# Optimization experiments

Hardware: AMD Instinct MI355X
Metric: run time of the kernel (lower is better)

## Reference

```python
import jax, jax.numpy as jnp
import numpy as np

BETA = 0.9
T = 16
THR = 1.0
SLOPE = 25.0  # snntorch surrogate.fast_sigmoid default slope


@jax.custom_vjp
def spike(x):
    # Heaviside forward, fast-sigmoid surrogate backward (snntorch fast_sigmoid)
    return (x > 0.0).astype(x.dtype)

def _spike_fwd(x):
    return spike(x), x

def _spike_bwd(x, g):
    return (g / (SLOPE * jnp.abs(x) + 1.0) ** 2,)

spike.defvjp(_spike_fwd, _spike_bwd)


def conv1d(x, w, b, pad):
    # x: (B, C_in, L), w: (C_out, C_in, K)
    y = jax.lax.conv_general_dilated(
        x, w, window_strides=(1,), padding=[(pad, pad)],
        dimension_numbers=("NCH", "OIH", "NCH"))
    return y + b[None, :, None]


def lif(cur, mem):
    # snntorch Leaky, reset_mechanism='subtract', threshold=1.0.
    # reset spike is computed from the PREVIOUS membrane and detached.
    reset = jax.lax.stop_gradient((mem > THR).astype(cur.dtype))
    mem = BETA * mem + cur - reset * THR
    spk = spike(mem - THR)
    return spk, mem


def setup_inputs() -> dict:
    key = jax.random.key(0)
    ks = jax.random.split(key, 14)

    def u(k, shape, fan_in):
        bound = 1.0 / np.sqrt(fan_in)
        return jax.random.uniform(k, shape, jnp.float32, -bound, bound)

    x = jax.random.normal(ks[0], (2048, 2, 128), dtype=jnp.float32)
    W1 = u(ks[1], (256, 2, 5), 2 * 5);    b1 = u(ks[2], (256,), 2 * 5)
    W2 = u(ks[3], (128, 256, 3), 256 * 3); b2 = u(ks[4], (128,), 256 * 3)
    W3 = u(ks[5], (64, 128, 3), 128 * 3);  b3 = u(ks[6], (64,), 128 * 3)
    W4 = u(ks[7], (2, 64, 3), 64 * 3);     b4 = u(ks[8], (2,), 64 * 3)
    fw1 = u(ks[9], (100, 256), 256);       fb1 = u(ks[10], (100,), 256)
    fw2 = u(ks[11], (40, 100), 100);       fb2 = u(ks[12], (40,), 100)
    return {"x": x, "W1": W1, "b1": b1, "W2": W2, "b2": b2,
            "W3": W3, "b3": b3, "W4": W4, "b4": b4,
            "fw1": fw1, "fb1": fb1, "fw2": fw2, "fb2": fb2}


def reference(x, W1, b1, W2, b2, W3, b3, W4, b4, fw1, fb1, fw2, fb2):
    B, _, L = x.shape
    f32 = x.dtype
    # conv1 input is constant across timesteps -> hoist (same math)
    cur1 = conv1d(x, W1, b1, 2)
    init = (jnp.zeros((B, 256, L), f32), jnp.zeros((B, 128, L), f32),
            jnp.zeros((B, 64, L), f32), jnp.zeros((B, 2, L), f32),
            jnp.zeros((B, 100), f32), jnp.zeros((B, 40), f32))

    def step(carry, _):
        m1, m2, m3, m4, m5, acc = carry
        s1, m1 = lif(cur1, m1)
        s2, m2 = lif(conv1d(s1, W2, b2, 1), m2)
        s3, m3 = lif(conv1d(s2, W3, b3, 1), m3)
        s4, m4 = lif(conv1d(s3, W4, b4, 1), m4)
        flat = s4.reshape(B, -1)                      # (B, 256)
        s5, m5 = lif(flat @ fw1.T + fb1, m5)
        acc = acc + s5 @ fw2.T + fb2
        return (m1, m2, m3, m4, m5, acc), None

    (_, _, _, _, _, acc), _ = jax.lax.scan(step, init, None, length=T)
    return acc / T
```

## Files before the change

### kernel.cpp

```cpp
#include <hip/hip_runtime.h>
#include <stdint.h>

#define BETA 0.9f

typedef unsigned short u16;
typedef unsigned char u8;
typedef _Float16 f16x8 __attribute__((ext_vector_type(8)));
typedef float f32x4 __attribute__((ext_vector_type(4)));

__device__ __forceinline__ void async_copy16(const void* g, void* l) {
  __builtin_amdgcn_global_load_lds(
      (const __attribute__((address_space(1))) uint32_t*)g,
      (__attribute__((address_space(3))) uint32_t*)l, 16, 0, 0);
}

__device__ __forceinline__ f16x8 expandB(uint32_t byte) {
  union { uint32_t u[4]; f16x8 v; } r;
  uint32_t z = byte | (byte << 15);
#pragma unroll
  for (int m = 0; m < 4; ++m)
    r.u[m] = ((z >> (2 * m)) & 0x10001u) << 12;
  return r.v;
}

__global__ void prep_kernel(const float* __restrict__ W2, const float* __restrict__ W3,
                            const float* __restrict__ fw1, const float* __restrict__ fw2,
                            u16* __restrict__ A2c, u16* __restrict__ A3c,
                            float* __restrict__ fw1T, float* __restrict__ fw2T) {
  int o = blockIdx.x * 256 + threadIdx.x;
  if (o < 98304) {
    int tap = o >> 15, r = o & 32767, co = r >> 8, ci = r & 255;
    float w = W2[(co * 256 + ci) * 3 + tap];
    float h = (float)(_Float16)w;
    _Float16 hv = (_Float16)(h * 2048.0f);
    _Float16 mv = (_Float16)((w - h) * 2048.0f);
    u16 hb, mb;
    __builtin_memcpy(&hb, &hv, 2);
    __builtin_memcpy(&mb, &mv, 2);
    int c = ci >> 5, cl = ci & 31;
    A2c[(((c * 2 + 0) * 3 + tap) * 128 + co) * 32 + cl] = hb;
    A2c[(((c * 2 + 1) * 3 + tap) * 128 + co) * 32 + cl] = mb;
  }
  int o2 = o - 98304;
  if (o2 >= 0 && o2 < 24576) {
    int tap = o2 >> 13, r = o2 & 8191, co = r >> 7, ci = r & 127;
    float w = W3[(co * 128 + ci) * 3 + tap];
    float h = (float)(_Float16)w;
    _Float16 hv = (_Float16)(h * 2048.0f);
    _Float16 mv = (_Float16)((w - h) * 2048.0f);
    u16 hb, mb;
    __builtin_memcpy(&hb, &hv, 2);
    __builtin_memcpy(&mb, &mv, 2);
    int c = ci >> 5, cl = ci & 31;
    A3c[(((c * 2 + 0) * 3 + tap) * 64 + co) * 32 + cl] = hb;
    A3c[(((c * 2 + 1) * 3 + tap) * 64 + co) * 32 + cl] = mb;
  }
  int o3 = o - (98304 + 24576);
  if (o3 >= 0 && o3 < 25600) {
    int f = o3 / 100, i = o3 % 100;
    fw1T[o3] = fw1[i * 256 + f];
  }
  int o4 = o - (98304 + 24576 + 25600);
  if (o4 >= 0 && o4 < 4000) {
    int i = o4 / 40, j = o4 % 40;
    fw2T[o4] = fw2[j * 100 + i];
  }
}

__global__ __launch_bounds__(256) void conv1_lif_kernel(
    const float* __restrict__ x, const float* __restrict__ W1,
    const float* __restrict__ b1, u8* __restrict__ SBT2) {
  __shared__ float xl[2][132];
  __shared__ u16 bl[8][128];
  int b = blockIdx.x, g = blockIdx.y;
  int tid = threadIdx.x;
  for (int i = tid; i < 264; i += 256) {
    int ci = i / 132, idx = i % 132, lg = idx - 2;
    xl[ci][idx] = (lg >= 0 && lg < 128) ? x[(b * 2 + ci) * 128 + lg] : 0.0f;
  }
  __syncthreads();
  int cosub = tid >> 5, tx = tid & 31;
  int co = g * 8 + cosub;
  float w[2][5];
#pragma unroll
  for (int ci = 0; ci < 2; ++ci)
#pragma unroll
    for (int k = 0; k < 5; ++k) w[ci][k] = W1[(co * 2 + ci) * 5 + k];
  float bias = b1[co];
  float cur[4];
#pragma unroll
  for (int j = 0; j < 4; ++j) {
    float acc = bias;
#pragma unroll
    for (int ci = 0; ci < 2; ++ci)
#pragma unroll
      for (int k = 0; k < 5; ++k) acc += w[ci][k] * xl[ci][4 * tx + j + k];
    cur[j] = acc;
  }
  float m[4] = {0.f, 0.f, 0.f, 0.f}, sp[4] = {0.f, 0.f, 0.f, 0.f};
  uint32_t bits[4] = {0u, 0u, 0u, 0u};
#pragma unroll
  for (int t = 0; t < 16; ++t) {
#pragma unroll
    for (int j = 0; j < 4; ++j) {
      m[j] = BETA * m[j] + cur[j] - sp[j];
      bool s = m[j] > 1.0f;
      bits[j] |= ((uint32_t)s) << t;
      sp[j] = s ? 1.0f : 0.0f;
    }
  }
#pragma unroll
  for (int j = 0; j < 4; ++j) bl[cosub][4 * tx + j] = (u16)bits[j];
  __syncthreads();
  if (tid < 128) {
    int l = tid;
    uint32_t wv[8];
#pragma unroll
    for (int j = 0; j < 8; ++j) wv[j] = bl[j][l];
    uint32_t ov[4];
#pragma unroll
    for (int k = 0; k < 4; ++k) {
      uint32_t v = 0;
#pragma unroll
      for (int tt = 0; tt < 4; ++tt) {
        int t = k * 4 + tt;
        uint32_t by = 0;
#pragma unroll
        for (int j = 0; j < 8; ++j) by |= ((wv[j] >> t) & 1u) << j;
        v |= by << (8 * tt);
      }
      ov[k] = v;
    }
    *(uint4*)(SBT2 + ((size_t)(b * 128 + l) * 32 + g) * 16) =
        make_uint4(ov[0], ov[1], ov[2], ov[3]);
  }
}

template <int CIN, int COUT, bool SBTOUT>
__global__ __launch_bounds__(256, 3) void conv_mfma_kernel(
    const u8* __restrict__ SBT, const u16* __restrict__ Agc,
    const float* __restrict__ bias, void* __restrict__ outp) {
  constexpr int NPHYS = CIN / 32;
  constexpr int NVIRT = 2 * NPHYS;
  constexpr int MT = COUT / 32;
  constexpr int GB = CIN / 8;
  constexpr int ABYTES = 3 * COUT * 32 * 2;
  constexpr int AW = ABYTES / 4;
  constexpr int AISS = AW / 1024;
  constexpr int EPB = 18432 + COUT * 8 * 2;
  constexpr int LDSSZ = (2 * ABYTES > EPB) ? 2 * ABYTES : EPB;
  __shared__ __align__(16) char lds[LDSSZ];

  int b = blockIdx.x, lb = blockIdx.y * 8;
  int tid = threadIdx.x, lane = tid & 63, wid = tid >> 6;
  int wx = wid & 1, wy = wid >> 1;
  int q = lane >> 4, xx = lane & 15;
  int mbase = wy * (COUT / 2);
  int lw = lb + wx * 4;

  f32x4 acc[MT][4];
#pragma unroll
  for (int mt = 0; mt < MT; ++mt)
#pragma unroll
    for (int nt = 0; nt < 4; ++nt) acc[mt][nt] = (f32x4){0.f, 0.f, 0.f, 0.f};

  uint32_t byt[6];
#pragma unroll
  for (int u = 0; u < 6; ++u) {
    int l_in = lw + u - 1;
    byt[u] = ((unsigned)l_in < 128u)
                 ? (uint32_t)SBT[((size_t)(b * 128 + l_in) * GB + q) * 16 + xx]
                 : 0u;
  }
  {
    const char* gsrc = (const char*)Agc + (size_t)wid * AW + lane * 16;
    char* ldst = lds + wid * AW;
#pragma unroll
    for (int i = 0; i < AISS; ++i) async_copy16(gsrc + i * 1024, ldst + i * 1024);
  }

  f16x8 Bf[6];
#pragma unroll 2
  for (int v = 0; v < NVIRT; ++v) {
    __syncthreads();
    if (v + 1 < NVIRT) {
      const char* gsrc = (const char*)Agc + (size_t)(v + 1) * ABYTES +
                         (size_t)wid * AW + lane * 16;
      char* ldst = lds + ((v + 1) & 1) * ABYTES + wid * AW;
#pragma unroll
      for (int i = 0; i < AISS; ++i) async_copy16(gsrc + i * 1024, ldst + i * 1024);
    }
    if ((v & 1) == 0) {
#pragma unroll
      for (int u = 0; u < 6; ++u) Bf[u] = expandB(byt[u]);
      int pn = (v >> 1) + 1;
      if (pn < NPHYS) {
#pragma unroll
        for (int u = 0; u < 6; ++u) {
          int l_in = lw + u - 1;
          byt[u] = ((unsigned)l_in < 128u)
                       ? (uint32_t)SBT[((size_t)(b * 128 + l_in) * GB + pn * 4 + q) * 16 + xx]
                       : 0u;
        }
      }
    }
    const u16* Asv = (const u16*)(lds + (v & 1) * ABYTES);
#pragma unroll
    for (int tap = 0; tap < 3; ++tap)
#pragma unroll
      for (int mt = 0; mt < MT; ++mt) {
        f16x8 Af = *(const f16x8*)(Asv + ((size_t)(tap * COUT + mbase + mt * 16 + xx)) * 32 + q * 8);
#pragma unroll
        for (int nt = 0; nt < 4; ++nt)
          acc[mt][nt] = __builtin_amdgcn_mfma_f32_16x16x32_f16(
              Af, Bf[nt + tap], acc[mt][nt], 0, 0, 0);
      }
  }
  __syncthreads();

  float* scr = (float*)(void*)lds + wid * 1152;
  u16* bl = (u16*)(lds + 18432);
#pragma unroll
  for (int mt = 0; mt < MT; ++mt) {
#pragma unroll
    for (int nt = 0; nt < 4; ++nt)
#pragma unroll
      for (int r = 0; r < 4; ++r)
        scr[(nt * 16 + q * 4 + r) * 18 + xx] = acc[mt][nt][r];
    __syncthreads();
    int co = mbase + mt * 16 + xx;
    float bc = bias[co];
    const float* rowp = scr + (q * 16 + xx) * 18;
    float mm = 0.f, sp = 0.f;
    uint32_t bits = 0;
#pragma unroll
    for (int t = 0; t < 16; ++t) {
      float cur = rowp[t] + bc;
      mm = BETA * mm + cur - sp;
      bool s = mm > 1.0f;
      bits |= ((uint32_t)s) << t;
      sp = s ? 1.0f : 0.0f;
    }
    bl[co * 8 + wx * 4 + q] = (u16)bits;
    __syncthreads();
  }

  if constexpr (SBTOUT) {
    constexpr int GBo = COUT / 8;
    if (tid < GBo * 8) {
      int g = tid & (GBo - 1), ll = tid / GBo;
      uint32_t wv[8];
#pragma unroll
      for (int j = 0; j < 8; ++j) wv[j] = bl[(8 * g + j) * 8 + ll];
      uint32_t ov[4];
#pragma unroll
      for (int k = 0; k < 4; ++k) {
        uint32_t v = 0;
#pragma unroll
        for (int tt = 0; tt < 4; ++tt) {
          int t = k * 4 + tt;
          uint32_t by = 0;
#pragma unroll
          for (int j = 0; j < 8; ++j) by |= ((wv[j] >> t) & 1u) << j;
          v |= by << (8 * tt);
        }
        ov[k] = v;
      }
      *(uint4*)((u8*)outp + ((size_t)(b * 128 + lb + ll) * GBo + g) * 16) =
          make_uint4(ov[0], ov[1], ov[2], ov[3]);
    }
  } else {
    if (tid < COUT) {
      uint4 v = *(const uint4*)(bl + tid * 8);
      *(uint4*)((u16*)outp + ((size_t)b * COUT + tid) * 128 + lb) = v;
    }
  }
}

__global__ __launch_bounds__(256) void head_kernel(
    const u16* __restrict__ s3bits, const float* __restrict__ W4,
    const float* __restrict__ b4, const float* __restrict__ fw1T,
    const float* __restrict__ fb1, const float* __restrict__ fw2T,
    const float* __restrict__ fb2, float* __restrict__ out) {
  __shared__ u16 s3l[64][130];
  __shared__ float W4l[384];
  __shared__ u16 flat4[256];
  __shared__ u16 s5b[100];
  int b = blockIdx.x, tid = threadIdx.x;

  for (int i = tid; i < 64 * 130; i += 256) {
    int ci = i / 130, idx = i % 130, lg = idx - 1;
    s3l[ci][idx] = (lg >= 0 && lg < 128) ? s3bits[((size_t)b * 64 + ci) * 128 + lg] : (u16)0;
  }
  for (int i = tid; i < 384; i += 256) W4l[i] = W4[i];
  __syncthreads();

  {
    int co = tid >> 7, l = tid & 127;
    float acc4[16];
#pragma unroll
    for (int t = 0; t < 16; ++t) acc4[t] = 0.f;
    for (int ci = 0; ci < 64; ++ci) {
#pragma unroll
      for (int k = 0; k < 3; ++k) {
        float wv = W4l[(co * 64 + ci) * 3 + k];
        uint32_t msk = s3l[ci][l + k];
#pragma unroll
        for (int t = 0; t < 16; ++t)
          acc4[t] = fmaf(wv, (float)((msk >> t) & 1u), acc4[t]);
      }
    }
    float bc = b4[co];
    float m = 0.f, sp = 0.f;
    uint32_t bits = 0;
#pragma unroll
    for (int t = 0; t < 16; ++t) {
      m = BETA * m + (acc4[t] + bc) - sp;
      bool s = m > 1.0f;
      bits |= ((uint32_t)s) << t;
      sp = s ? 1.0f : 0.0f;
    }
    flat4[tid] = (u16)bits;
  }
  __syncthreads();

  if (tid < 100) {
    float acc5[16];
#pragma unroll
    for (int t = 0; t < 16; ++t) acc5[t] = 0.f;
    for (int f = 0; f < 256; ++f) {
      float wv = fw1T[f * 100 + tid];
      uint32_t msk = flat4[f];
#pragma unroll
      for (int t = 0; t < 16; ++t)
        acc5[t] = fmaf(wv, (float)((msk >> t) & 1u), acc5[t]);
    }
    float bc = fb1[tid];
    float m = 0.f, sp = 0.f;
    uint32_t bits = 0;
#pragma unroll
    for (int t = 0; t < 16; ++t) {
      m = BETA * m + (acc5[t] + bc) - sp;
      bool s = m > 1.0f;
      bits |= ((uint32_t)s) << t;
      sp = s ? 1.0f : 0.0f;
    }
    s5b[tid] = (u16)bits;
  }
  __syncthreads();

  if (tid < 40) {
    float a = 0.f;
    for (int i = 0; i < 100; ++i) {
      float wv = fw2T[i * 40 + tid];
      a = fmaf(wv, (float)__popc((uint32_t)s5b[i]), a);
    }
    out[b * 40 + tid] = a * 0.0625f + fb2[tid];
  }
}

extern "C" void kernel_launch(void* const* d_in, const int* in_sizes, int n_in,
                              void* d_out, int out_size, void* d_ws, size_t ws_size,
                              hipStream_t stream) {
  const float* x   = (const float*)d_in[0];
  const float* W1  = (const float*)d_in[1];
  const float* b1  = (const float*)d_in[2];
  const float* W2  = (const float*)d_in[3];
  const float* b2  = (const float*)d_in[4];
  const float* W3  = (const float*)d_in[5];
  const float* b3  = (const float*)d_in[6];
  const float* W4  = (const float*)d_in[7];
  const float* b4  = (const float*)d_in[8];
  const float* fw1 = (const float*)d_in[9];
  const float* fb1 = (const float*)d_in[10];
  const float* fw2 = (const float*)d_in[11];
  const float* fb2 = (const float*)d_in[12];
  float* out = (float*)d_out;

  char* ws = (char*)d_ws;
  u16*   A2c  = (u16*)(ws);
  u16*   A3c  = (u16*)(ws + 393216);
  float* fw1T = (float*)(ws + 491520);
  float* fw2T = (float*)(ws + 593920);
  u8*    SBT2 = (u8*)(ws + 610304);
  u8*    SBT3 = (u8*)(ws + 610304 + 134217728);
  u16*   s3b  = (u16*)(ws + 610304 + 134217728 + 67108864);

  prep_kernel<<<dim3(596), dim3(256), 0, stream>>>(W2, W3, fw1, fw2, A2c, A3c, fw1T, fw2T);
  conv1_lif_kernel<<<dim3(2048, 32), dim3(256), 0, stream>>>(x, W1, b1, SBT2);
  conv_mfma_kernel<256, 128, true><<<dim3(2048, 16), dim3(256), 0, stream>>>(SBT2, A2c, b2, SBT3);
  conv_mfma_kernel<128, 64, false><<<dim3(2048, 16), dim3(256), 0, stream>>>(SBT3, A3c, b3, s3b);
  head_kernel<<<dim3(2048), dim3(256), 0, stream>>>(s3b, W4, b4, fw1T, fb1, fw2T, fb2, out);
}
```

Measured before the change: 2.025 ms.

## Switch conv MFMA from split-fp16 to three-limb int8 MFMA with binary spikes

Replaces the two-term fp16 weight split (hi+residual) and f16 MFMA with a three-limb int8 fixed-point decomposition of the weights and i32 16x16x64 int8 MFMA, since spike inputs are 0/1. Accumulators are shifted left by 7 bits between limbs and rescaled by 2^-25 at the end. This doubles the K per MFMA and halves the weight bytes per limb, but now does three passes instead of two and fully unrolls the channel loop. It also repacks spike bytes into int8 lanes and changes the weight layout, and the fixed-point scheme risks precision or overflow differences near the threshold.

```diff
diff --git a/kernel.cpp b/kernel.cpp
--- a/kernel.cpp
+++ b/kernel.cpp
@@ -5,8 +5,8 @@
 
 typedef unsigned short u16;
 typedef unsigned char u8;
-typedef _Float16 f16x8 __attribute__((ext_vector_type(8)));
-typedef float f32x4 __attribute__((ext_vector_type(4)));
+typedef signed char i8;
+typedef int i32x4 __attribute__((ext_vector_type(4)));
 
 __device__ __forceinline__ void async_copy16(const void* g, void* l) {
   __builtin_amdgcn_global_load_lds(
@@ -14,46 +14,39 @@
       (__attribute__((address_space(3))) uint32_t*)l, 16, 0, 0);
 }
 
-__device__ __forceinline__ f16x8 expandB(uint32_t byte) {
-  union { uint32_t u[4]; f16x8 v; } r;
-  uint32_t z = byte | (byte << 15);
-#pragma unroll
-  for (int m = 0; m < 4; ++m)
-    r.u[m] = ((z >> (2 * m)) & 0x10001u) << 12;
-  return r.v;
-}
-
 __global__ void prep_kernel(const float* __restrict__ W2, const float* __restrict__ W3,
                             const float* __restrict__ fw1, const float* __restrict__ fw2,
-                            u16* __restrict__ A2c, u16* __restrict__ A3c,
+                            i8* __restrict__ A2c, i8* __restrict__ A3c,
                             float* __restrict__ fw1T, float* __restrict__ fw2T) {
   int o = blockIdx.x * 256 + threadIdx.x;
   if (o < 98304) {
     int tap = o >> 15, r = o & 32767, co = r >> 8, ci = r & 255;
     float w = W2[(co * 256 + ci) * 3 + tap];
-    float h = (float)(_Float16)w;
-    _Float16 hv = (_Float16)(h * 2048.0f);
-    _Float16 mv = (_Float16)((w - h) * 2048.0f);
-    u16 hb, mb;
-    __builtin_memcpy(&hb, &hv, 2);
-    __builtin_memcpy(&mb, &mv, 2);
-    int c = ci >> 5, cl = ci & 31;
-    A2c[(((c * 2 + 0) * 3 + tap) * 128 + co) * 32 + cl] = hb;
-    A2c[(((c * 2 + 1) * 3 + tap) * 128 + co) * 32 + cl] = mb;
+    float d0 = __builtin_rintf(w * 0x1p11f);
+    float r1 = w - d0 * 0x1p-11f;
+    float d1 = __builtin_rintf(r1 * 0x1p18f);
+    float r2 = r1 - d1 * 0x1p-18f;
+    float d2 = __builtin_rintf(r2 * 0x1p25f);
+    int phys = ci >> 6, cl = ci & 63;
+    int base = ((phys * 3 + tap) * 128 + co) * 64 + cl;
+    A2c[base] = (i8)(int)d0;
+    A2c[98304 + base] = (i8)(int)d1;
+    A2c[196608 + base] = (i8)(int)d2;
   }
   int o2 = o - 98304;
   if (o2 >= 0 && o2 < 24576) {
     int tap = o2 >> 13, r = o2 & 8191, co = r >> 7, ci = r & 127;
     float w = W3[(co * 128 + ci) * 3 + tap];
-    float h = (float)(_Float16)w;
-    _Float16 hv = (_Float16)(h * 2048.0f);
-    _Float16 mv = (_Float16)((w - h) * 2048.0f);
-    u16 hb, mb;
-    __builtin_memcpy(&hb, &hv, 2);
-    __builtin_memcpy(&mb, &mv, 2);
-    int c = ci >> 5, cl = ci & 31;
-    A3c[(((c * 2 + 0) * 3 + tap) * 64 + co) * 32 + cl] = hb;
-    A3c[(((c * 2 + 1) * 3 + tap) * 64 + co) * 32 + cl] = mb;
+    float d0 = __builtin_rintf(w * 0x1p11f);
+    float r1 = w - d0 * 0x1p-11f;
+    float d1 = __builtin_rintf(r1 * 0x1p18f);
+    float r2 = r1 - d1 * 0x1p-18f;
+    float d2 = __builtin_rintf(r2 * 0x1p25f);
+    int phys = ci >> 6, cl = ci & 63;
+    int base = ((phys * 3 + tap) * 64 + co) * 64 + cl;
+    A3c[base] = (i8)(int)d0;
+    A3c[24576 + base] = (i8)(int)d1;
+    A3c[49152 + base] = (i8)(int)d2;
   }
   int o3 = o - (98304 + 24576);
   if (o3 >= 0 && o3 < 25600) {
@@ -136,20 +129,26 @@
   }
 }
 
+template <int GB>
+__device__ __forceinline__ uint32_t ldpair(const u8* rowbase, int l_in, int off) {
+  if ((unsigned)l_in >= 128u) return 0u;
+  const u8* p = rowbase + (size_t)l_in * (GB * 16) + off;
+  uint32_t a = p[0], b2 = p[16];
+  return a | (b2 << 8);
+}
+
 template <int CIN, int COUT, bool SBTOUT>
 __global__ __launch_bounds__(256, 3) void conv_mfma_kernel(
-    const u8* __restrict__ SBT, const u16* __restrict__ Agc,
+    const u8* __restrict__ SBT, const i8* __restrict__ Agc,
     const float* __restrict__ bias, void* __restrict__ outp) {
-  constexpr int NPHYS = CIN / 32;
-  constexpr int NVIRT = 2 * NPHYS;
+  constexpr int NPHYS = CIN / 64;
+  constexpr int NVIRT = 3 * NPHYS;
   constexpr int MT = COUT / 32;
   constexpr int GB = CIN / 8;
-  constexpr int ABYTES = 3 * COUT * 32 * 2;
+  constexpr int ABYTES = 3 * COUT * 64;
   constexpr int AW = ABYTES / 4;
   constexpr int AISS = AW / 1024;
-  constexpr int EPB = 18432 + COUT * 8 * 2;
-  constexpr int LDSSZ = (2 * ABYTES > EPB) ? 2 * ABYTES : EPB;
-  __shared__ __align__(16) char lds[LDSSZ];
+  __shared__ __align__(16) char lds[2 * ABYTES];
 
   int b = blockIdx.x, lb = blockIdx.y * 8;
   int tid = threadIdx.x, lane = tid & 63, wid = tid >> 6;
@@ -158,19 +157,21 @@
   int mbase = wy * (COUT / 2);
   int lw = lb + wx * 4;
 
-  f32x4 acc[MT][4];
+  i32x4 acc[MT][4];
 #pragma unroll
   for (int mt = 0; mt < MT; ++mt)
 #pragma unroll
-    for (int nt = 0; nt < 4; ++nt) acc[mt][nt] = (f32x4){0.f, 0.f, 0.f, 0.f};
-
-  uint32_t byt[6];
-#pragma unroll
-  for (int u = 0; u < 6; ++u) {
-    int l_in = lw + u - 1;
-    byt[u] = ((unsigned)l_in < 128u)
-                 ? (uint32_t)SBT[((size_t)(b * 128 + l_in) * GB + q) * 16 + xx]
-                 : 0u;
+    for (int nt = 0; nt < 4; ++nt) acc[mt][nt] = (i32x4){0, 0, 0, 0};
+
+  const u8* rowbase = SBT + (size_t)b * 128 * GB * 16;
+  int boff = 32 * q + xx;
+
+  uint32_t bpk[NPHYS][3];
+#pragma unroll
+  for (int j = 0; j < 3; ++j) {
+    uint32_t lo = ldpair<GB>(rowbase, lw + 2 * j - 1, boff);
+    uint32_t hi = ldpair<GB>(rowbase, lw + 2 * j, boff);
+    bpk[0][j] = lo | (hi << 16);
   }
   {
     const char* gsrc = (const char*)Agc + (size_t)wid * AW + lane * 16;
@@ -179,9 +180,9 @@
     for (int i = 0; i < AISS; ++i) async_copy16(gsrc + i * 1024, ldst + i * 1024);
   }
 
-  f16x8 Bf[6];
-#pragma unroll 2
+#pragma unroll
   for (int v = 0; v < NVIRT; ++v) {
+    const int c = v % NPHYS;
     __syncthreads();
     if (v + 1 < NVIRT) {
       const char* gsrc = (const char*)Agc + (size_t)(v + 1) * ABYTES +
@@ -190,47 +191,57 @@
 #pragma unroll
       for (int i = 0; i < AISS; ++i) async_copy16(gsrc + i * 1024, ldst + i * 1024);
     }
-    if ((v & 1) == 0) {
-#pragma unroll
-      for (int u = 0; u < 6; ++u) Bf[u] = expandB(byt[u]);
-      int pn = (v >> 1) + 1;
-      if (pn < NPHYS) {
-#pragma unroll
-        for (int u = 0; u < 6; ++u) {
-          int l_in = lw + u - 1;
-          byt[u] = ((unsigned)l_in < 128u)
-                       ? (uint32_t)SBT[((size_t)(b * 128 + l_in) * GB + pn * 4 + q) * 16 + xx]
-                       : 0u;
-        }
+    if (v + 1 < NPHYS) {
+#pragma unroll
+      for (int j = 0; j < 3; ++j) {
+        uint32_t lo = ldpair<GB>(rowbase, lw + 2 * j - 1, 128 * (v + 1) + boff);
+        uint32_t hi = ldpair<GB>(rowbase, lw + 2 * j, 128 * (v + 1) + boff);
+        bpk[v + 1][j] = lo | (hi << 16);
       }
     }
-    const u16* Asv = (const u16*)(lds + (v & 1) * ABYTES);
+    if (v == NPHYS || v == 2 * NPHYS) {
+#pragma unroll
+      for (int mt = 0; mt < MT; ++mt)
+#pragma unroll
+        for (int nt = 0; nt < 4; ++nt) acc[mt][nt] = acc[mt][nt] << 7;
+    }
+    i32x4 Bf[6];
+#pragma unroll
+    for (int u = 0; u < 6; ++u) {
+      uint32_t sel = (bpk[c][u >> 1] >> ((u & 1) * 16)) & 0xFFFFu;
+      uint32_t b0 = sel & 0xFFu, b1 = sel >> 8;
+      Bf[u].x = (int)(((b0 & 0xFu) * 0x204081u) & 0x01010101u);
+      Bf[u].y = (int)(((b0 >> 4) * 0x204081u) & 0x01010101u);
+      Bf[u].z = (int)(((b1 & 0xFu) * 0x204081u) & 0x01010101u);
+      Bf[u].w = (int)(((b1 >> 4) * 0x204081u) & 0x01010101u);
+    }
+    const i8* Asv = (const i8*)(lds + (v & 1) * ABYTES);
 #pragma unroll
     for (int tap = 0; tap < 3; ++tap)
 #pragma unroll
       for (int mt = 0; mt < MT; ++mt) {
-        f16x8 Af = *(const f16x8*)(Asv + ((size_t)(tap * COUT + mbase + mt * 16 + xx)) * 32 + q * 8);
+        i32x4 Af = *(const i32x4*)(Asv + (tap * COUT + mbase + mt * 16 + xx) * 64 + q * 16);
 #pragma unroll
         for (int nt = 0; nt < 4; ++nt)
-          acc[mt][nt] = __builtin_amdgcn_mfma_f32_16x16x32_f16(
+          acc[mt][nt] = __builtin_amdgcn_mfma_i32_16x16x64_i8(
               Af, Bf[nt + tap], acc[mt][nt], 0, 0, 0);
       }
   }
   __syncthreads();
 
-  float* scr = (float*)(void*)lds + wid * 1152;
-  u16* bl = (u16*)(lds + 18432);
+  float* scr = (float*)(void*)lds + wid * 1216;
+  u16* bl = (u16*)(lds + 19456);
 #pragma unroll
   for (int mt = 0; mt < MT; ++mt) {
 #pragma unroll
     for (int nt = 0; nt < 4; ++nt)
 #pragma unroll
       for (int r = 0; r < 4; ++r)
-        scr[(nt * 16 + q * 4 + r) * 18 + xx] = acc[mt][nt][r];
+        scr[(nt * 16 + q * 4 + r) * 19 + xx] = (float)acc[mt][nt][r] * 0x1p-25f;
     __syncthreads();
     int co = mbase + mt * 16 + xx;
     float bc = bias[co];
-    const float* rowp = scr + (q * 16 + xx) * 18;
+    const float* rowp = scr + (q * 16 + xx) * 19;
     float mm = 0.f, sp = 0.f;
     uint32_t bits = 0;
 #pragma unroll
@@ -378,13 +389,13 @@
   float* out = (float*)d_out;
 
   char* ws = (char*)d_ws;
-  u16*   A2c  = (u16*)(ws);
-  u16*   A3c  = (u16*)(ws + 393216);
-  float* fw1T = (float*)(ws + 491520);
-  float* fw2T = (float*)(ws + 593920);
-  u8*    SBT2 = (u8*)(ws + 610304);
-  u8*    SBT3 = (u8*)(ws + 610304 + 134217728);
-  u16*   s3b  = (u16*)(ws + 610304 + 134217728 + 67108864);
+  i8*    A2c  = (i8*)(ws);
+  i8*    A3c  = (i8*)(ws + 294912);
+  float* fw1T = (float*)(ws + 368640);
+  float* fw2T = (float*)(ws + 471040);
+  u8*    SBT2 = (u8*)(ws + 487424);
+  u8*    SBT3 = (u8*)(ws + 487424 + 134217728);
+  u16*   s3b  = (u16*)(ws + 487424 + 134217728 + 67108864);
 
   prep_kernel<<<dim3(596), dim3(256), 0, stream>>>(W2, W3, fw1, fw2, A2c, A3c, fw1T, fw2T);
   conv1_lif_kernel<<<dim3(2048, 32), dim3(256), 0, stream>>>(x, W1, b1, SBT2);
```

After: 2.510 ms. 1.24x slower.
